# Kernel optimization log

Hardware: AMD Instinct MI355X
Metric: run time of the kernel (lower is better)

## Reference

```python
import jax, jax.numpy as jnp
import numpy as np

B, L, C, S, W, R = 2, 16, 64, 64, 128, 32
MOD_HIDDEN = 32


def _conv3d(x, k, b, pad_hw):
    # x: (B,C,L,S,W), k: (O,I,1,kh,kw)
    y = jax.lax.conv_general_dilated(
        x, k, window_strides=(1, 1, 1),
        padding=((0, 0), (pad_hw, pad_hw), (pad_hw, pad_hw)),
        dimension_numbers=('NCDHW', 'OIDHW', 'NCDHW'))
    return y + b[None, :, None, None, None]


def setup_inputs() -> dict:
    key = jax.random.key(0)
    ks = jax.random.split(key, 16)
    d = {}
    d['x'] = jax.random.normal(ks[0], (B, L, C, S, W), jnp.float32)
    u1 = jax.random.uniform(ks[1], (C, R), jnp.float32)
    u2 = jax.random.uniform(ks[2], (C, R), jnp.float32)
    r_min, r_max = 0.8, 0.99
    d['nu_log'] = jnp.log(-0.5 * jnp.log(u1 * (r_max ** 2 - r_min ** 2) + r_min ** 2))
    d['theta_log'] = jnp.log(u2 * jnp.float32(2 * np.pi))
    d['disp_nu'] = jnp.zeros((C, R), jnp.float32)
    d['disp_theta'] = jnp.zeros((C, R), jnp.float32)
    d['mlp_w1'] = jax.random.normal(ks[3], (C, MOD_HIDDEN), jnp.float32) / np.sqrt(C).astype(np.float32)
    d['mlp_b1'] = jnp.zeros((MOD_HIDDEN,), jnp.float32)
    d['mlp_w2'] = jax.random.normal(ks[4], (MOD_HIDDEN, C * R * 2), jnp.float32) / np.sqrt(MOD_HIDDEN).astype(np.float32)
    d['mlp_b2'] = jnp.zeros((C * R * 2,), jnp.float32)
    d['forcing_scale'] = jnp.float32(0.1)
    d['U_row_r'] = jax.random.normal(ks[5], (C, S, R), jnp.float32) / np.sqrt(S).astype(np.float32)
    d['U_row_i'] = jax.random.normal(ks[6], (C, S, R), jnp.float32) / np.sqrt(S).astype(np.float32)
    d['V_col_r'] = jax.random.normal(ks[7], (C, W, R), jnp.float32) / np.sqrt(W).astype(np.float32)
    d['V_col_i'] = jax.random.normal(ks[8], (C, W, R), jnp.float32) / np.sqrt(W).astype(np.float32)
    d['proj_W_r'] = jax.random.normal(ks[9], (C, C), jnp.float32) / np.sqrt(C).astype(np.float32)
    d['proj_W_i'] = jax.random.normal(ks[10], (C, C), jnp.float32) / np.sqrt(C).astype(np.float32)
    d['proj_b_r'] = jnp.zeros((C,), jnp.float32)
    d['proj_b_i'] = jnp.zeros((C,), jnp.float32)
    fan = np.sqrt(C * 9).astype(np.float32)
    d['convr_k'] = jax.random.normal(ks[11], (C, C, 1, 3, 3), jnp.float32) / fan
    d['convr_b'] = jnp.zeros((C,), jnp.float32)
    d['convi_k'] = jax.random.normal(ks[12], (C, C, 1, 3, 3), jnp.float32) / fan
    d['convi_b'] = jnp.zeros((C,), jnp.float32)
    d['fuse_k'] = jax.random.normal(ks[13], (C, 2 * C, 1, 1, 1), jnp.float32) / np.sqrt(2 * C).astype(np.float32)
    d['fuse_b'] = jnp.zeros((C,), jnp.float32)
    d['ln_g'] = jnp.ones((S, W), jnp.float32)
    d['ln_b'] = jnp.zeros((S, W), jnp.float32)
    return d


def reference(x, nu_log, theta_log, disp_nu, disp_theta, mlp_w1, mlp_b1,
              mlp_w2, mlp_b2, forcing_scale, U_row_r, U_row_i, V_col_r,
              V_col_i, proj_W_r, proj_W_i, proj_b_r, proj_b_i, convr_k,
              convr_b, convi_k, convi_b, fuse_k, fuse_b, ln_g, ln_b):
    # Diagonal LRU poles lam = exp(-exp(nu) + i*exp(theta)), per (C,R)
    nu = jnp.exp(nu_log + disp_nu)
    theta = jnp.exp(theta_log + disp_theta)
    lam = jnp.exp(jax.lax.complex(-nu, theta))
    gamma = jnp.sqrt(jnp.clip(1.0 - jnp.abs(lam) ** 2, 1e-6, None))

    # Selective input-dependent forcing from spatially-pooled context
    ctx = x.mean(axis=(-2, -1))  # (B,L,C)
    f = jnp.tanh(ctx @ mlp_w1 + mlp_b1) @ mlp_w2 + mlp_b2
    f = f.reshape(ctx.shape[0], ctx.shape[1], C, R, 2)
    forcing = forcing_scale * jax.lax.complex(f[..., 0], f[..., 1])  # (B,L,C,R)

    # Low-rank complex spatial projection to rank-R state per channel
    U = jax.lax.complex(U_row_r, U_row_i)  # (C,S,R)
    V = jax.lax.complex(V_col_r, V_col_i)  # (C,W,R)
    xc = x.astype(jnp.complex64)
    u = jnp.einsum('blcsw,csr->blcwr', xc, jnp.conj(U))
    u = jnp.einsum('blcwr,cwr->blcr', u, jnp.conj(V))  # (B,L,C,R)
    u = gamma * u * (1.0 + forcing)

    # Diagonal linear recurrence h_t = lam*h_{t-1} + u_t via associative scan over L
    A = jnp.broadcast_to(lam[None, None], u.shape)

    def comb(e1, e2):
        a1, b1 = e1
        a2, b2 = e2
        return a1 * a2, a2 * b1 + b2

    _, h = jax.lax.associative_scan(comb, (A, u), axis=1)

    # Reconstruct spatial field from low-rank states
    t = jnp.einsum('blcr,csr->blcsr', h, U)
    y = jnp.einsum('blcsr,cwr->blcsw', t, V)  # (B,L,C,S,W) complex

    projW = jax.lax.complex(proj_W_r, proj_W_i)
    projb = jax.lax.complex(proj_b_r, proj_b_i)
    y = jnp.einsum('blcsw,oc->blosw', y, projW) + projb[None, None, :, None, None]

    # Post-recurrence spatial convs on real/imag parts, fuse, layernorm, residual
    yr = jnp.transpose(jnp.real(y), (0, 2, 1, 3, 4))  # (B,C,L,S,W)
    yi = jnp.transpose(jnp.imag(y), (0, 2, 1, 3, 4))
    yr = _conv3d(yr, convr_k, convr_b, 1)
    yi = _conv3d(yi, convi_k, convi_b, 1)
    fused = _conv3d(jnp.concatenate([yr, yi], axis=1), fuse_k, fuse_b, 0)
    fused = jnp.transpose(fused, (0, 2, 1, 3, 4))  # (B,L,C,S,W)

    mu = fused.mean(axis=(-2, -1), keepdims=True)
    var = fused.var(axis=(-2, -1), keepdims=True)
    normed = (fused - mu) / jnp.sqrt(var + 1e-5) * ln_g + ln_b
    return normed + x
```

## Files before the change

kernel.cpp:

```cpp
#include <hip/hip_runtime.h>

typedef unsigned short u16;
typedef unsigned int u32;
typedef __attribute__((ext_vector_type(8))) short short8;
typedef __attribute__((ext_vector_type(4))) float f32x4;

constexpr int B = 2, L = 16, C = 64, S = 64, W = 128, R = 32, MH = 32;
constexpr int BL = B * L;
constexpr int SW = S * W;
constexpr int CR = C * R;
constexpr int F2 = C * R * 2;

__device__ __forceinline__ float us2f(u16 h) { return __uint_as_float(((u32)h) << 16); }
__device__ __forceinline__ float bf_lo(u32 u) { return __uint_as_float(u << 16); }
__device__ __forceinline__ float bf_hi(u32 u) { return __uint_as_float(u & 0xffff0000u); }
__device__ __forceinline__ u16 f2bu(float f) {
  u32 u = __float_as_uint(f);
  u32 r = (u + 0x7fffu + ((u >> 16) & 1u)) >> 16;
  return (u16)r;
}
__device__ __forceinline__ u32 pack2(float lo, float hi) {
  return (u32)f2bu(lo) | ((u32)f2bu(hi) << 16);
}

__global__ void k_prep(const float* __restrict__ nu_log, const float* __restrict__ th_log,
                       const float* __restrict__ dnu, const float* __restrict__ dth,
                       float* __restrict__ lamr, float* __restrict__ lami,
                       float* __restrict__ gam) {
  int i = blockIdx.x * 256 + threadIdx.x;
  if (i >= CR) return;
  float nu = expf(nu_log[i] + dnu[i]);
  float th = expf(th_log[i] + dth[i]);
  float mag = expf(-nu);
  lamr[i] = mag * cosf(th);
  lami[i] = mag * sinf(th);
  gam[i] = sqrtf(fmaxf(1.0f - mag * mag, 1e-6f));
}

__global__ void k_keff(const float* __restrict__ fuse_k, const float* __restrict__ fuse_b,
                       const float* __restrict__ convr_k, const float* __restrict__ convr_b,
                       const float* __restrict__ convi_k, const float* __restrict__ convi_b,
                       u16* __restrict__ keff_bf, float* __restrict__ biaseff) {
  int i = blockIdx.x * 256 + threadIdx.x;
  if (i < C * 2 * C * 9) {
    int o = i / (2 * C * 9);
    int rem = i - o * (2 * C * 9);
    int cin2 = rem / 9;
    int seg = rem - cin2 * 9;
    const float* ck = (cin2 < C) ? convr_k : convi_k;
    int cin = cin2 & (C - 1);
    int fbase = o * 2 * C + ((cin2 < C) ? 0 : C);
    float acc = 0.f;
    for (int m = 0; m < C; ++m)
      acc += fuse_k[fbase + m] * ck[(m * C + cin) * 9 + seg];
    int kstep = cin2 >> 5;
    int kk = cin2 & 31;
    int lane = (o & 15) | ((kk >> 3) << 4);
    int j = kk & 7;
    int m_tile = o >> 4;
    keff_bf[((((seg * 4 + kstep) * 4 + m_tile) * 64 + lane) << 3) + j] = f2bu(acc);
  } else if (i < C * 2 * C * 9 + C) {
    int o = i - C * 2 * C * 9;
    float acc = fuse_b[o];
    for (int m = 0; m < C; ++m) {
      acc += fuse_k[o * 2 * C + m] * convr_b[m];
      acc += fuse_k[o * 2 * C + C + m] * convi_b[m];
    }
    biaseff[o] = acc;
  }
}

__global__ void k_apack(const float* __restrict__ pWr, const float* __restrict__ pWi,
                        u16* __restrict__ aproj) {
  int i = blockIdx.x * 256 + threadIdx.x;
  if (i >= 128 * 128) return;
  int m = i >> 7, k = i & 127;
  int c = k >> 1, im = k & 1;
  int o = m & 63;
  float v;
  if (m < 64) v = im ? -pWi[o * 64 + c] : pWr[o * 64 + c];
  else        v = im ?  pWr[o * 64 + c] : pWi[o * 64 + c];
  aproj[i] = f2bu(v);
}

__global__ __launch_bounds__(256) void k_mlp(
    const float* __restrict__ ctx, const float* __restrict__ w1, const float* __restrict__ b1,
    const float* __restrict__ w2, const float* __restrict__ b2, const float* __restrict__ fscale,
    float* __restrict__ forcing) {
  int bl = blockIdx.x >> 4;
  int kt = blockIdx.x & 15;
  int k0 = kt * 256;
  __shared__ float cv[C];
  __shared__ float hid[MH];
  __shared__ float lw2[MH * 256];
  int t = threadIdx.x;
  if (t < C) cv[t] = ctx[bl * C + t];
  for (int i = t; i < MH * 64; i += 256) {
    int j = i >> 6, q = i & 63;
    ((float4*)lw2)[i] = ((const float4*)(w2 + (size_t)j * F2 + k0))[q];
  }
  __syncthreads();
  if (t < MH) {
    float a = b1[t];
    for (int c2 = 0; c2 < C; ++c2) a += cv[c2] * w1[c2 * MH + t];
    hid[t] = tanhf(a);
  }
  __syncthreads();
  float scale = fscale[0];
  float a = b2[k0 + t];
#pragma unroll
  for (int j = 0; j < MH; ++j) a += hid[j] * lw2[j * 256 + t];
  forcing[(size_t)bl * F2 + k0 + t] = scale * a;
}

__global__ __launch_bounds__(256) void k_enc(
    const float* __restrict__ x,
    const float* __restrict__ Vr, const float* __restrict__ Vi,
    const float* __restrict__ Ur, const float* __restrict__ Ui,
    float* __restrict__ ctx, float* __restrict__ u) {
  int blc = blockIdx.x;
  int c = blc & (C - 1);
  __shared__ __align__(16) char smem[17408 * 2 + 16384 + 64];
  u16* xt = (u16*)smem;
  u16* bt = (u16*)(smem + 17408);
  float* uldr = (float*)(smem + 34816);
  float* uldi = uldr + 2048;
  float* y1  = (float*)smem;
  float* part = (float*)(smem + 17408);
  float* red = (float*)(smem + 17408 * 2 + 16384);
  int t = threadIdx.x;
  int lane = t & 63, wv = t >> 6;
  float sm = 0.f;
  {
    const float4* xp = (const float4*)(x + (size_t)blc * SW);
    for (int i = t; i < SW / 4; i += 256) {
      float4 v = xp[i];
      sm += v.x + v.y + v.z + v.w;
      int idx = i * 4, s = idx >> 7, w = idx & 127;
      u32* d = (u32*)&xt[s * 136 + w];
      d[0] = pack2(v.x, v.y);
      d[1] = pack2(v.z, v.w);
    }
  }
#pragma unroll
  for (int o = 32; o > 0; o >>= 1) sm += __shfl_down(sm, o, 64);
  if (lane == 0) red[wv] = sm;
  {
    const float* vrp = Vr + (size_t)c * 4096;
    const float* vip = Vi + (size_t)c * 4096;
    for (int i = t; i < 4096; i += 256) {
      int w = i >> 5, r = i & 31;
      bt[r * 136 + w]        = f2bu(vrp[i]);
      bt[(32 + r) * 136 + w] = f2bu(-vip[i]);
    }
  }
  {
    const float* urp = Ur + (size_t)c * 2048;
    const float* uip = Ui + (size_t)c * 2048;
    for (int i = t; i < 2048; i += 256) { uldr[i] = urp[i]; uldi[i] = uip[i]; }
  }
  __syncthreads();
  if (t == 0) ctx[blc] = (red[0] + red[1] + red[2] + red[3]) * (1.f / SW);
  int quad = lane >> 4, l15 = lane & 15;
  f32x4 zf = {0.f, 0.f, 0.f, 0.f};
  f32x4 acc[4] = {zf, zf, zf, zf};
#pragma unroll
  for (int ks = 0; ks < 4; ++ks) {
    int kofs = ks * 32 + quad * 8;
    short8 bf = *(const short8*)&bt[(wv * 16 + l15) * 136 + kofs];
#pragma unroll
    for (int mt = 0; mt < 4; ++mt) {
      short8 af = *(const short8*)&xt[(mt * 16 + l15) * 136 + kofs];
      acc[mt] = __builtin_amdgcn_mfma_f32_16x16x32_bf16(af, bf, acc[mt], 0, 0, 0);
    }
  }
  __syncthreads();
#pragma unroll
  for (int mt = 0; mt < 4; ++mt)
#pragma unroll
    for (int reg = 0; reg < 4; ++reg)
      y1[(mt * 16 + quad * 4 + reg) * 65 + wv * 16 + l15] = acc[mt][reg];
  __syncthreads();
  {
    int r = t & 31, sg = t >> 5;
    float pr = 0.f, pi = 0.f;
#pragma unroll
    for (int k = 0; k < 8; ++k) {
      int s = sg * 8 + k;
      float yr = y1[s * 65 + r], yi = y1[s * 65 + 32 + r];
      float ur = uldr[s * 32 + r], ui = uldi[s * 32 + r];
      pr += ur * yr + ui * yi;
      pi += ur * yi - ui * yr;
    }
    part[sg * 64 + r * 2]     = pr;
    part[sg * 64 + r * 2 + 1] = pi;
  }
  __syncthreads();
  if (t < 32) {
    float pr = 0.f, pi = 0.f;
#pragma unroll
    for (int sg = 0; sg < 8; ++sg) {
      pr += part[sg * 64 + t * 2];
      pi += part[sg * 64 + t * 2 + 1];
    }
    u[((size_t)blc * R + t) * 2]     = pr;
    u[((size_t)blc * R + t) * 2 + 1] = pi;
  }
}

__global__ void k_scan(const float* __restrict__ lamr, const float* __restrict__ lami,
                       const float* __restrict__ gam, const float* __restrict__ forcing,
                       const float* __restrict__ u, float* __restrict__ h) {
  int i = blockIdx.x * 256 + threadIdx.x;
  if (i >= B * CR) return;
  int b = i / CR;
  int cr = i - b * CR;
  float lr = lamr[cr], li = lami[cr], g = gam[cr];
  float hr = 0.f, hi = 0.f;
  for (int l = 0; l < L; ++l) {
    size_t off = ((size_t)(b * L + l) * CR + cr) * 2;
    float ur0 = u[off], ui0 = u[off + 1];
    float fr = forcing[off], fi = forcing[off + 1];
    float ofr = 1.f + fr;
    float ur = g * (ur0 * ofr - ui0 * fi);
    float ui = g * (ur0 * fi + ui0 * ofr);
    float nr = lr * hr - li * hi + ur;
    float ni = lr * hi + li * hr + ui;
    hr = nr; hi = ni;
    h[off] = hr; h[off + 1] = hi;
  }
}

__global__ __launch_bounds__(256) void k_decode(
    const float* __restrict__ h,
    const float* __restrict__ Ur, const float* __restrict__ Ui,
    const float* __restrict__ Vr, const float* __restrict__ Vi,
    u32* __restrict__ y_cm32, int bl_base) {
  int bid = blockIdx.x;
  int c = bid & 63;
  int blh = bid >> 6;
  int bl = bl_base + blh;
  __shared__ __align__(16) u16 ldA[64 * 72];
  __shared__ __align__(16) u16 ldBr[128 * 72];
  __shared__ __align__(16) u16 ldBi[128 * 72];
  int t = threadIdx.x;
  {
    const float* hp = h + ((size_t)(bl * C + c) * R) * 2;
    const float* urp = Ur + (size_t)c * (S * R);
    const float* uip = Ui + (size_t)c * (S * R);
    for (int p = t; p < S * R; p += 256) {
      int s = p >> 5, r = p & 31;
      float hr = hp[r * 2], hi = hp[r * 2 + 1];
      float ur = urp[p], ui = uip[p];
      ldA[s * 72 + r]      = f2bu(hr * ur - hi * ui);
      ldA[s * 72 + 32 + r] = f2bu(hr * ui + hi * ur);
    }
  }
  {
    const float* vrp = Vr + (size_t)c * (W * R);
    const float* vip = Vi + (size_t)c * (W * R);
    for (int p = t; p < W * R; p += 256) {
      int w = p >> 5, r = p & 31;
      float vr = vrp[p], vi = vip[p];
      ldBr[w * 72 + r]      = f2bu(vr);
      ldBr[w * 72 + 32 + r] = f2bu(-vi);
      ldBi[w * 72 + r]      = f2bu(vi);
      ldBi[w * 72 + 32 + r] = f2bu(vr);
    }
  }
  __syncthreads();
  int lane = t & 63, q = t >> 6;
  int quad = lane >> 4, l15 = lane & 15;
  f32x4 zf = {0.f, 0.f, 0.f, 0.f};
  f32x4 accr[4][2], acci[4][2];
#pragma unroll
  for (int mt = 0; mt < 4; ++mt)
#pragma unroll
    for (int nt = 0; nt < 2; ++nt) { accr[mt][nt] = zf; acci[mt][nt] = zf; }
#pragma unroll
  for (int ks = 0; ks < 2; ++ks) {
    int kofs = ks * 32 + quad * 8;
    short8 af[4];
#pragma unroll
    for (int mt = 0; mt < 4; ++mt)
      af[mt] = *(const short8*)&ldA[(mt * 16 + l15) * 72 + kofs];
#pragma unroll
    for (int nt = 0; nt < 2; ++nt) {
      int wrow = q * 32 + nt * 16 + l15;
      short8 br = *(const short8*)&ldBr[wrow * 72 + kofs];
      short8 bi = *(const short8*)&ldBi[wrow * 72 + kofs];
#pragma unroll
      for (int mt = 0; mt < 4; ++mt) {
        accr[mt][nt] = __builtin_amdgcn_mfma_f32_16x16x32_bf16(af[mt], br, accr[mt][nt], 0, 0, 0);
        acci[mt][nt] = __builtin_amdgcn_mfma_f32_16x16x32_bf16(af[mt], bi, acci[mt][nt], 0, 0, 0);
      }
    }
  }
  u32* dst = y_cm32 + ((size_t)(blh * 64 + c) << 13);
#pragma unroll
  for (int mt = 0; mt < 4; ++mt) {
#pragma unroll
    for (int nt = 0; nt < 2; ++nt) {
      int w = q * 32 + nt * 16 + l15;
#pragma unroll
      for (int reg = 0; reg < 4; ++reg) {
        int s = mt * 16 + quad * 4 + reg;
        dst[s * 128 + w] = pack2(accr[mt][nt][reg], acci[mt][nt][reg]);
      }
    }
  }
}

__global__ __launch_bounds__(256) void k_proj(
    const u32* __restrict__ y_cm32, const u16* __restrict__ aproj,
    const float* __restrict__ pbr, const float* __restrict__ pbi,
    u16* __restrict__ ynhwc, int bl_base) {
  int bid = blockIdx.x;
  int ntile = bid & 15;
  int blh = bid >> 4;
  int bl = bl_base + blh;
  __shared__ __align__(16) u16 lda[128 * 136];
  __shared__ __align__(16) u32 ldb[128 * 68];
  __shared__ float ldbias[128];
  int t = threadIdx.x;
  for (int i = t; i < 128 * 16; i += 256) {
    int m = i >> 4, qq = i & 15;
    ((uint4*)&lda[m * 136])[qq] = ((const uint4*)&aproj[m * 128])[qq];
  }
  if (t < 128) ldbias[t] = t < 64 ? pbr[t] : pbi[t - 64];

  int lane = t & 63, wv = t >> 6;
  int quad = lane >> 4, l15 = lane & 15;
  int cidx = t & 63, seg = t >> 6;
  f32x4 zf = {0.f, 0.f, 0.f, 0.f};

  for (int chunk = 0; chunk < 4; ++chunk) {
    int n0 = ntile * 512 + chunk * 128;
    __syncthreads();
    {
      const uint4* src = (const uint4*)(y_cm32 + (((size_t)(blh * 64 + cidx)) << 13) + n0 + seg * 32);
      u32 tmp[32];
#pragma unroll
      for (int qq = 0; qq < 8; ++qq) {
        uint4 v = src[qq];
        tmp[qq * 4] = v.x; tmp[qq * 4 + 1] = v.y; tmp[qq * 4 + 2] = v.z; tmp[qq * 4 + 3] = v.w;
      }
#pragma unroll
      for (int j = 0; j < 32; ++j)
        ldb[(seg * 32 + j) * 68 + cidx] = tmp[j];
    }
    __syncthreads();
    f32x4 acc[8][2];
#pragma unroll
    for (int mt = 0; mt < 8; ++mt) { acc[mt][0] = zf; acc[mt][1] = zf; }
    const u16* ldb16 = (const u16*)ldb;
#pragma unroll
    for (int ks = 0; ks < 4; ++ks) {
      int kofs = ks * 32 + quad * 8;
      short8 af[8];
#pragma unroll
      for (int mt = 0; mt < 8; ++mt)
        af[mt] = *(const short8*)&lda[(mt * 16 + l15) * 136 + kofs];
#pragma unroll
      for (int nt = 0; nt < 2; ++nt) {
        int nrow = wv * 32 + nt * 16 + l15;
        short8 bf = *(const short8*)&ldb16[nrow * 136 + kofs];
#pragma unroll
        for (int mt = 0; mt < 8; ++mt)
          acc[mt][nt] = __builtin_amdgcn_mfma_f32_16x16x32_bf16(af[mt], bf, acc[mt][nt], 0, 0, 0);
      }
    }
#pragma unroll
    for (int nt = 0; nt < 2; ++nt) {
      int n = n0 + wv * 32 + nt * 16 + l15;
      u16* drow = ynhwc + (((size_t)bl * SW + n) << 7);
#pragma unroll
      for (int mt = 0; mt < 8; ++mt) {
        int ch = mt * 16 + quad * 4;
        u32 lo = pack2(acc[mt][nt][0] + ldbias[ch],     acc[mt][nt][1] + ldbias[ch + 1]);
        u32 hi = pack2(acc[mt][nt][2] + ldbias[ch + 2], acc[mt][nt][3] + ldbias[ch + 3]);
        u32* dp = (u32*)(drow + ch);
        dp[0] = lo; dp[1] = hi;
      }
    }
  }
}

__global__ __launch_bounds__(256) void k_conv(
    const u16* __restrict__ ynhwc, const u16* __restrict__ keff_bf,
    const float* __restrict__ biaseff, u16* __restrict__ fused) {
  int bid = blockIdx.x;
  int wt = bid & 3;
  int st = (bid >> 2) & 31;
  int bl = bid >> 7;
  int s0 = st * 2;
  int w0 = wt * 32;
  __shared__ __align__(16) u16 win[4][34][136];
  int t = threadIdx.x;
  int c_lo = (w0 == 0) ? 1 : 0;
  int c_hi = (w0 == 96) ? 33 : 34;
  uint4 z4 = make_uint4(0u, 0u, 0u, 0u);
  for (int rr = 0; rr < 4; ++rr) {
    int rs = s0 - 1 + rr;
    if (rs < 0 || rs >= S) {
      uint4* wrow = (uint4*)&win[rr][0][0];
      for (int i = t; i < 578; i += 256) wrow[i] = z4;
    } else {
      if (w0 == 0 && t < 16) ((uint4*)&win[rr][0][0])[t] = z4;
      if (w0 == 96 && t < 16) ((uint4*)&win[rr][33][0])[t] = z4;
      const uint4* src = (const uint4*)(ynhwc + (((size_t)bl * S + rs) * W + (w0 - 1 + c_lo)) * 128);
      int n4 = (c_hi - c_lo) * 16;
      for (int i = t; i < n4; i += 256) {
        int col = i >> 4, q = i & 15;
        ((uint4*)&win[rr][c_lo + col][0])[q] = src[i];
      }
    }
  }
  __syncthreads();

  int lane = t & 63;
  int wv = t >> 6;
  int mp = wv & 1;
  int np = wv >> 1;
  int quad = lane >> 4, l15 = lane & 15;
  int chq = quad * 8;

  f32x4 zf = {0.f, 0.f, 0.f, 0.f};
  f32x4 acc00 = zf, acc01 = zf, acc10 = zf, acc11 = zf;
  const short8* ap = (const short8*)keff_bf;

  for (int seg = 0; seg < 9; ++seg) {
    int dr = seg / 3;
    int dc = seg - dr * 3;
    const u16* b0base = &win[np + dr][l15 + dc][chq];
    const u16* b1base = b0base + 16 * 136;
#pragma unroll
    for (int ks = 0; ks < 4; ++ks) {
      short8 a0 = ap[((seg * 4 + ks) * 4 + 2 * mp) * 64 + lane];
      short8 a1 = ap[((seg * 4 + ks) * 4 + 2 * mp + 1) * 64 + lane];
      short8 b0 = *(const short8*)(b0base + ks * 32);
      short8 b1 = *(const short8*)(b1base + ks * 32);
      acc00 = __builtin_amdgcn_mfma_f32_16x16x32_bf16(a0, b0, acc00, 0, 0, 0);
      acc01 = __builtin_amdgcn_mfma_f32_16x16x32_bf16(a0, b1, acc01, 0, 0, 0);
      acc10 = __builtin_amdgcn_mfma_f32_16x16x32_bf16(a1, b0, acc10, 0, 0, 0);
      acc11 = __builtin_amdgcn_mfma_f32_16x16x32_bf16(a1, b1, acc11, 0, 0, 0);
    }
  }

  int s_out = s0 + np;
#pragma unroll
  for (int mi = 0; mi < 2; ++mi) {
    f32x4 aN0 = mi ? acc10 : acc00;
    f32x4 aN1 = mi ? acc11 : acc01;
#pragma unroll
    for (int reg = 0; reg < 4; ++reg) {
      int o = (2 * mp + mi) * 16 + quad * 4 + reg;
      float bias = biaseff[o];
      size_t rowoff = ((size_t)(bl * C + o) * S + s_out) * W;
      fused[rowoff + w0 + l15]      = f2bu(aN0[reg] + bias);
      fused[rowoff + w0 + 16 + l15] = f2bu(aN1[reg] + bias);
    }
  }
}

__global__ __launch_bounds__(256) void k_ln(
    const u16* __restrict__ fused,
    const float* __restrict__ ln_g, const float* __restrict__ ln_b,
    const float* __restrict__ x, float* __restrict__ out) {
  int blc = blockIdx.x;
  __shared__ u16 fs[SW];
  __shared__ float red[12];
  int t = threadIdx.x;
  const uint4* fp = (const uint4*)(fused + (size_t)blc * SW);
  float sm = 0.f, sq = 0.f;
  for (int i = t; i < SW / 8; i += 256) {
    uint4 v = fp[i];
    ((uint4*)fs)[i] = v;
    float f0 = bf_lo(v.x), f1 = bf_hi(v.x), f2 = bf_lo(v.y), f3 = bf_hi(v.y);
    float f4 = bf_lo(v.z), f5 = bf_hi(v.z), f6 = bf_lo(v.w), f7 = bf_hi(v.w);
    sm += f0 + f1 + f2 + f3 + f4 + f5 + f6 + f7;
    sq += f0 * f0 + f1 * f1 + f2 * f2 + f3 * f3 + f4 * f4 + f5 * f5 + f6 * f6 + f7 * f7;
  }
#pragma unroll
  for (int off = 32; off > 0; off >>= 1) {
    sm += __shfl_down(sm, off, 64);
    sq += __shfl_down(sq, off, 64);
  }
  int lane = t & 63, wid = t >> 6;
  if (lane == 0) { red[wid * 2] = sm; red[wid * 2 + 1] = sq; }
  __syncthreads();
  if (t == 0) {
    float S1 = red[0] + red[2] + red[4] + red[6];
    float S2 = red[1] + red[3] + red[5] + red[7];
    float mu = S1 * (1.f / SW);
    float var = S2 * (1.f / SW) - mu * mu;
    red[8] = mu;
    red[9] = rsqrtf(var + 1e-5f);
  }
  __syncthreads();
  float mu = red[8], rstd = red[9];
  const float* xp = x + (size_t)blc * SW;
  float* op = out + (size_t)blc * SW;
  for (int i = t; i < SW; i += 256)
    op[i] = (us2f(fs[i]) - mu) * rstd * ln_g[i] + ln_b[i] + xp[i];
}

extern "C" void kernel_launch(void* const* d_in, const int* in_sizes, int n_in,
                              void* d_out, int out_size, void* d_ws, size_t ws_size,
                              hipStream_t stream) {
  (void)in_sizes; (void)n_in; (void)out_size; (void)ws_size;
  const float* x       = (const float*)d_in[0];
  const float* nu_log  = (const float*)d_in[1];
  const float* th_log  = (const float*)d_in[2];
  const float* dnu     = (const float*)d_in[3];
  const float* dth     = (const float*)d_in[4];
  const float* w1      = (const float*)d_in[5];
  const float* b1      = (const float*)d_in[6];
  const float* w2      = (const float*)d_in[7];
  const float* b2      = (const float*)d_in[8];
  const float* fscale  = (const float*)d_in[9];
  const float* Ur      = (const float*)d_in[10];
  const float* Ui      = (const float*)d_in[11];
  const float* Vr      = (const float*)d_in[12];
  const float* Vi      = (const float*)d_in[13];
  const float* pWr     = (const float*)d_in[14];
  const float* pWi     = (const float*)d_in[15];
  const float* pbr     = (const float*)d_in[16];
  const float* pbi     = (const float*)d_in[17];
  const float* convr_k = (const float*)d_in[18];
  const float* convr_b = (const float*)d_in[19];
  const float* convi_k = (const float*)d_in[20];
  const float* convi_b = (const float*)d_in[21];
  const float* fuse_k  = (const float*)d_in[22];
  const float* fuse_b  = (const float*)d_in[23];
  const float* ln_g    = (const float*)d_in[24];
  const float* ln_b    = (const float*)d_in[25];
  float* out = (float*)d_out;

  char* ws = (char*)d_ws;
  float* lamr    = (float*)ws;
  float* lami    = lamr + 2048;
  float* gam     = lami + 2048;
  float* biaseff = gam + 2048;
  float* ctx     = biaseff + 64;
  float* forcing = ctx + 2048;
  float* ubuf    = forcing + 131072;
  float* hbuf    = ubuf + 131072;
  u16* keff_bf   = (u16*)(hbuf + 131072);
  u16* aproj     = keff_bf + 73728;
  size_t off = ((size_t)((char*)(aproj + 16384) - ws) + 255) & ~(size_t)255;
  u32* y_cm32    = (u32*)(ws + off);
  u16* fused     = (u16*)y_cm32;
  u16* ynhwc     = (u16*)(ws + off + (size_t)32 * 1024 * 1024);

  k_prep<<<8, 256, 0, stream>>>(nu_log, th_log, dnu, dth, lamr, lami, gam);
  k_keff<<<289, 256, 0, stream>>>(fuse_k, fuse_b, convr_k, convr_b, convi_k, convi_b,
                                  keff_bf, biaseff);
  k_apack<<<64, 256, 0, stream>>>(pWr, pWi, aproj);
  k_enc<<<BL * C, 256, 0, stream>>>(x, Vr, Vi, Ur, Ui, ctx, ubuf);
  k_mlp<<<BL * 16, 256, 0, stream>>>(ctx, w1, b1, w2, b2, fscale, forcing);
  k_scan<<<16, 256, 0, stream>>>(lamr, lami, gam, forcing, ubuf, hbuf);
  k_decode<<<1024, 256, 0, stream>>>(hbuf, Ur, Ui, Vr, Vi, y_cm32, 0);
  k_proj<<<256, 256, 0, stream>>>(y_cm32, aproj, pbr, pbi, ynhwc, 0);
  k_decode<<<1024, 256, 0, stream>>>(hbuf, Ur, Ui, Vr, Vi, y_cm32, 16);
  k_proj<<<256, 256, 0, stream>>>(y_cm32, aproj, pbr, pbi, ynhwc, 16);
  k_conv<<<4096, 256, 0, stream>>>(ynhwc, keff_bf, biaseff, fused);
  k_ln<<<BL * C, 256, 0, stream>>>(fused, ln_g, ln_b, x, out);
}
```

Before: 365.4 us.

## Split conv input channels into two halves to halve LDS window and raise occupancy

The conv kernel now loads the 128-channel input window in two 64-channel passes, which halves the shared memory tile from 4x34x136 to 4x34x72 bf16. It also adds a launch-bounds occupancy hint of 8 blocks. The smaller LDS footprint is meant to let more blocks reside per CU and hide load latency. The cost is an extra global load pass and an extra barrier per block, plus a row stride change that may shift LDS bank-conflict behaviour.

```diff
diff --git a/kernel.cpp b/kernel.cpp
--- a/kernel.cpp
+++ b/kernel.cpp
@@ -386,7 +386,7 @@
   }
 }
 
-__global__ __launch_bounds__(256) void k_conv(
+__global__ __launch_bounds__(256, 8) void k_conv(
     const u16* __restrict__ ynhwc, const u16* __restrict__ keff_bf,
     const float* __restrict__ biaseff, u16* __restrict__ fused) {
   int bid = blockIdx.x;
@@ -395,28 +395,11 @@
   int bl = bid >> 7;
   int s0 = st * 2;
   int w0 = wt * 32;
-  __shared__ __align__(16) u16 win[4][34][136];
+  __shared__ __align__(16) u16 win[4][34][72];
   int t = threadIdx.x;
   int c_lo = (w0 == 0) ? 1 : 0;
   int c_hi = (w0 == 96) ? 33 : 34;
   uint4 z4 = make_uint4(0u, 0u, 0u, 0u);
-  for (int rr = 0; rr < 4; ++rr) {
-    int rs = s0 - 1 + rr;
-    if (rs < 0 || rs >= S) {
-      uint4* wrow = (uint4*)&win[rr][0][0];
-      for (int i = t; i < 578; i += 256) wrow[i] = z4;
-    } else {
-      if (w0 == 0 && t < 16) ((uint4*)&win[rr][0][0])[t] = z4;
-      if (w0 == 96 && t < 16) ((uint4*)&win[rr][33][0])[t] = z4;
-      const uint4* src = (const uint4*)(ynhwc + (((size_t)bl * S + rs) * W + (w0 - 1 + c_lo)) * 128);
-      int n4 = (c_hi - c_lo) * 16;
-      for (int i = t; i < n4; i += 256) {
-        int col = i >> 4, q = i & 15;
-        ((uint4*)&win[rr][c_lo + col][0])[q] = src[i];
-      }
-    }
-  }
-  __syncthreads();
 
   int lane = t & 63;
   int wv = t >> 6;
@@ -426,39 +409,65 @@
   int chq = quad * 8;
 
   f32x4 zf = {0.f, 0.f, 0.f, 0.f};
-  f32x4 acc00 = zf, acc01 = zf, acc10 = zf, acc11 = zf;
+  f32x4 acc[2][2];
+  acc[0][0] = zf; acc[0][1] = zf; acc[1][0] = zf; acc[1][1] = zf;
   const short8* ap = (const short8*)keff_bf;
 
-  for (int seg = 0; seg < 9; ++seg) {
-    int dr = seg / 3;
-    int dc = seg - dr * 3;
-    const u16* b0base = &win[np + dr][l15 + dc][chq];
-    const u16* b1base = b0base + 16 * 136;
-#pragma unroll
-    for (int ks = 0; ks < 4; ++ks) {
-      short8 a0 = ap[((seg * 4 + ks) * 4 + 2 * mp) * 64 + lane];
-      short8 a1 = ap[((seg * 4 + ks) * 4 + 2 * mp + 1) * 64 + lane];
-      short8 b0 = *(const short8*)(b0base + ks * 32);
-      short8 b1 = *(const short8*)(b1base + ks * 32);
-      acc00 = __builtin_amdgcn_mfma_f32_16x16x32_bf16(a0, b0, acc00, 0, 0, 0);
-      acc01 = __builtin_amdgcn_mfma_f32_16x16x32_bf16(a0, b1, acc01, 0, 0, 0);
-      acc10 = __builtin_amdgcn_mfma_f32_16x16x32_bf16(a1, b0, acc10, 0, 0, 0);
-      acc11 = __builtin_amdgcn_mfma_f32_16x16x32_bf16(a1, b1, acc11, 0, 0, 0);
+#pragma unroll
+  for (int p = 0; p < 2; ++p) {
+    if (p) __syncthreads();
+    for (int rr = 0; rr < 4; ++rr) {
+      int rs = s0 - 1 + rr;
+      if (rs < 0 || rs >= S) {
+        for (int i = t; i < 34 * 8; i += 256) {
+          int col = i >> 3, q = i & 7;
+          ((uint4*)&win[rr][col][0])[q] = z4;
+        }
+      } else {
+        if (w0 == 0 && t < 8) ((uint4*)&win[rr][0][0])[t] = z4;
+        if (w0 == 96 && t < 8) ((uint4*)&win[rr][33][0])[t] = z4;
+        const uint4* src = (const uint4*)(ynhwc +
+            (((size_t)bl * S + rs) * W + (w0 - 1 + c_lo)) * 128 + p * 64);
+        int n4 = (c_hi - c_lo) * 8;
+        for (int i = t; i < n4; i += 256) {
+          int col = i >> 3, q = i & 7;
+          ((uint4*)&win[rr][c_lo + col][0])[q] = src[col * 16 + q];
+        }
+      }
+    }
+    __syncthreads();
+
+#pragma unroll
+    for (int seg = 0; seg < 9; ++seg) {
+      const int dr = seg / 3;
+      const int dc = seg - dr * 3;
+      const u16* b0base = &win[np + dr][l15 + dc][0];
+      const u16* b1base = b0base + 16 * 72;
+#pragma unroll
+      for (int ks2 = 0; ks2 < 2; ++ks2) {
+        const int ks = p * 2 + ks2;
+        short8 a0 = ap[((seg * 4 + ks) * 4 + 2 * mp) * 64 + lane];
+        short8 a1 = ap[((seg * 4 + ks) * 4 + 2 * mp + 1) * 64 + lane];
+        short8 b0 = *(const short8*)(b0base + chq + ks2 * 32);
+        short8 b1 = *(const short8*)(b1base + chq + ks2 * 32);
+        acc[0][0] = __builtin_amdgcn_mfma_f32_16x16x32_bf16(a0, b0, acc[0][0], 0, 0, 0);
+        acc[0][1] = __builtin_amdgcn_mfma_f32_16x16x32_bf16(a0, b1, acc[0][1], 0, 0, 0);
+        acc[1][0] = __builtin_amdgcn_mfma_f32_16x16x32_bf16(a1, b0, acc[1][0], 0, 0, 0);
+        acc[1][1] = __builtin_amdgcn_mfma_f32_16x16x32_bf16(a1, b1, acc[1][1], 0, 0, 0);
+      }
     }
   }
 
   int s_out = s0 + np;
 #pragma unroll
   for (int mi = 0; mi < 2; ++mi) {
-    f32x4 aN0 = mi ? acc10 : acc00;
-    f32x4 aN1 = mi ? acc11 : acc01;
 #pragma unroll
     for (int reg = 0; reg < 4; ++reg) {
       int o = (2 * mp + mi) * 16 + quad * 4 + reg;
       float bias = biaseff[o];
       size_t rowoff = ((size_t)(bl * C + o) * S + s_out) * W;
-      fused[rowoff + w0 + l15]      = f2bu(aN0[reg] + bias);
-      fused[rowoff + w0 + 16 + l15] = f2bu(aN1[reg] + bias);
+      fused[rowoff + w0 + l15]      = f2bu(acc[mi][0][reg] + bias);
+      fused[rowoff + w0 + 16 + l15] = f2bu(acc[mi][1][reg] + bias);
     }
   }
 }
```

After: 374.1 us. 1.02x slower.
